# Optimization experiments

Measured on AMD Instinct MI355X. Metric: run time of the kernel, lower is better.

Reference implementation:

```python
import jax, jax.numpy as jnp
import numpy as np


def setup_inputs() -> dict:
    key = jax.random.key(0)
    k1, k2, k3, k4 = jax.random.split(key, 4)
    N, IN, OUT, R, B = 8192, 256, 256, 8, 4
    a = jax.random.normal(k1, (N, N), dtype=jnp.float32)
    x = jax.random.normal(k2, (N, IN, R), dtype=jnp.float32)
    w_bases = jax.random.normal(k3, (B, IN, OUT), dtype=jnp.float32) * (1.0 / np.sqrt(IN))
    w_rel = jax.random.normal(k4, (R, B), dtype=jnp.float32) * 0.5
    return {"a": a, "x": x, "w_bases": w_bases, "w_rel": w_rel}


def reference(a, x, w_bases, w_rel):
    # Basis-combined per-relation weights: [R, IN, OUT]
    w = jnp.einsum('rb,bio->rio', w_rel, w_bases)
    # Per-relation aggregation: support_r = a @ x[:, :, r] -> stack as [N, R, IN]
    # (matches torch.cat([a @ x[:,:,r] for r], dim=1) ordering)
    supports = jnp.einsum('nm,mir->nri', a, x)  # [N, R, IN]
    # tmp [N, R*IN] @ weights [R*IN, OUT] fused as one einsum
    out = jnp.einsum('nri,rio->no', supports, w)  # [N, OUT]
    return out
```

## Files before the change

kernel.cpp:

```cpp
#include <hip/hip_runtime.h>
#include <stdint.h>

typedef __fp16 f16x2 __attribute__((ext_vector_type(2)));
typedef __fp16 f16x8 __attribute__((ext_vector_type(8)));
typedef float  f32x4 __attribute__((ext_vector_type(4)));

#define GLOBAL_AS __attribute__((address_space(1)))
#define LDS_AS    __attribute__((address_space(3)))

#define NN   8192
#define INC  256
#define OUTC 256
#define K2   2048
#define YTN  ((size_t)OUTC * NN)

__device__ __forceinline__ void async_copy16(const void* g, void* l) {
    __builtin_amdgcn_global_load_lds((const GLOBAL_AS uint32_t*)g,
                                     (LDS_AS uint32_t*)l, 16, 0, 0);
}

__device__ __forceinline__ f16x8 cvt_f32x8_to_f16x8(f32x4 u0, f32x4 u1) {
    f16x8 out;
    f16x2* p = (f16x2*)&out;
    p[0] = __builtin_amdgcn_cvt_pkrtz(u0[0], u0[1]);
    p[1] = __builtin_amdgcn_cvt_pkrtz(u0[2], u0[3]);
    p[2] = __builtin_amdgcn_cvt_pkrtz(u1[0], u1[1]);
    p[3] = __builtin_amdgcn_cvt_pkrtz(u1[2], u1[3]);
    return out;
}

__global__ void build_w2t16(const float* __restrict__ wb, const float* __restrict__ wr,
                            __fp16* __restrict__ W2T16) {
    int o = blockIdx.x;
    int i = threadIdx.x;
    float s[8];
#pragma unroll
    for (int r = 0; r < 8; ++r) s[r] = 0.f;
#pragma unroll
    for (int b = 0; b < 4; ++b) {
        float w = wb[((size_t)((b << 8) + i)) * OUTC + o];
#pragma unroll
        for (int r = 0; r < 8; ++r) s[r] = fmaf(wr[r * 4 + b], w, s[r]);
    }
    f16x8 out;
    f16x2* p = (f16x2*)&out;
    p[0] = __builtin_amdgcn_cvt_pkrtz(s[0], s[1]);
    p[1] = __builtin_amdgcn_cvt_pkrtz(s[2], s[3]);
    p[2] = __builtin_amdgcn_cvt_pkrtz(s[4], s[5]);
    p[3] = __builtin_amdgcn_cvt_pkrtz(s[6], s[7]);
    *reinterpret_cast<f16x8*>(&W2T16[(size_t)o * K2 + i * 8]) = out;
}

__global__ __launch_bounds__(256, 2)
void gemm1_xstream(const __fp16* __restrict__ W2, const float* __restrict__ X,
                   float* __restrict__ Cp, int kPerSplit) {
    __shared__ __align__(16) __fp16 As[2][128 * 32];
    const int bm = blockIdx.x * 128;
    const int bn = blockIdx.y * 128;
    const int k0 = blockIdx.z * kPerSplit;

    const int tid  = threadIdx.x;
    const int lane = tid & 63;
    const int wave = tid >> 6;
    const int wm   = (wave >> 1) * 64;
    const int wn   = (wave & 1) * 64;
    const int quad = lane >> 4;
    const int l16  = lane & 15;

    f32x4 acc[4][4];
#pragma unroll
    for (int ti = 0; ti < 4; ++ti)
#pragma unroll
        for (int tj = 0; tj < 4; ++tj)
            acc[ti][tj] = (f32x4){0.f, 0.f, 0.f, 0.f};

    const int nt = kPerSplit / 32;
    int cur = 0;

    {
#pragma unroll
        for (int i = 0; i < 2; ++i) {
            int r0 = wave * 32 + i * 16;
            int r  = r0 + (lane >> 2);
            int c  = (lane & 3) ^ ((r >> 1) & 3);
            async_copy16(W2 + (size_t)(bm + r) * K2 + k0 + c * 8,
                         (char*)As[0] + r0 * 64);
        }
    }

    for (int t = 0; t < nt; ++t) {
        __syncthreads();
        if (t + 1 < nt) {
            int kc = k0 + (t + 1) * 32;
#pragma unroll
            for (int i = 0; i < 2; ++i) {
                int r0 = wave * 32 + i * 16;
                int r  = r0 + (lane >> 2);
                int c  = (lane & 3) ^ ((r >> 1) & 3);
                async_copy16(W2 + (size_t)(bm + r) * K2 + kc + c * 8,
                             (char*)As[cur ^ 1] + r0 * 64);
            }
        }
        const int kc = k0 + t * 32;

        f16x8 bf[4];
#pragma unroll
        for (int j = 0; j < 4; ++j) {
            const float* g = X + (size_t)(bn + wn + j * 16 + l16) * K2 + kc + quad * 8;
            f32x4 u0 = *(const f32x4*)g;
            f32x4 u1 = *(const f32x4*)(g + 4);
            bf[j] = cvt_f32x8_to_f16x8(u0, u1);
        }
        f16x8 af[4];
#pragma unroll
        for (int j = 0; j < 4; ++j) {
            int row = wm + j * 16 + l16;
            int p   = quad ^ ((row >> 1) & 3);
            af[j] = *(const f16x8*)(&As[cur][0] + row * 32 + p * 8);
        }
#pragma unroll
        for (int ti = 0; ti < 4; ++ti)
#pragma unroll
            for (int tj = 0; tj < 4; ++tj)
                acc[ti][tj] = __builtin_amdgcn_mfma_f32_16x16x32_f16(
                    af[ti], bf[tj], acc[ti][tj], 0, 0, 0);
        cur ^= 1;
    }

    float* Cz = Cp + (size_t)blockIdx.z * 256 * NN;
#pragma unroll
    for (int ti = 0; ti < 4; ++ti)
#pragma unroll
        for (int tj = 0; tj < 4; ++tj)
#pragma unroll
            for (int r = 0; r < 4; ++r) {
                int row = bm + wm + ti * 16 + quad * 4 + r;
                int col = bn + wn + tj * 16 + l16;
                Cz[(size_t)row * NN + col] = acc[ti][tj][r];
            }
}

__global__ __launch_bounds__(256, 2)
void gemm2_astream(const float* __restrict__ A, const __fp16* __restrict__ Y,
                   float* __restrict__ Cp, int kPerSplit) {
    __shared__ __align__(16) __fp16 Bs[2][256 * 32];
    const int bm = blockIdx.x * 128;
    const int k0 = blockIdx.z * kPerSplit;

    const int tid  = threadIdx.x;
    const int lane = tid & 63;
    const int wave = tid >> 6;
    const int wm   = (wave >> 1) * 64;
    const int wn   = (wave & 1) * 128;
    const int quad = lane >> 4;
    const int l16  = lane & 15;

    f32x4 acc[4][8];
#pragma unroll
    for (int ti = 0; ti < 4; ++ti)
#pragma unroll
        for (int tj = 0; tj < 8; ++tj)
            acc[ti][tj] = (f32x4){0.f, 0.f, 0.f, 0.f};

    const int nt = kPerSplit / 32;
    int cur = 0;

    {
#pragma unroll
        for (int i = 0; i < 4; ++i) {
            int r0 = wave * 64 + i * 16;
            int r  = r0 + (lane >> 2);
            int c  = (lane & 3) ^ ((r >> 1) & 3);
            async_copy16(Y + (size_t)r * NN + k0 + c * 8,
                         (char*)Bs[0] + r0 * 64);
        }
    }

    for (int t = 0; t < nt; ++t) {
        __syncthreads();
        if (t + 1 < nt) {
            int kc = k0 + (t + 1) * 32;
#pragma unroll
            for (int i = 0; i < 4; ++i) {
                int r0 = wave * 64 + i * 16;
                int r  = r0 + (lane >> 2);
                int c  = (lane & 3) ^ ((r >> 1) & 3);
                async_copy16(Y + (size_t)r * NN + kc + c * 8,
                             (char*)Bs[cur ^ 1] + r0 * 64);
            }
        }
        const int kc = k0 + t * 32;

        f16x8 af[4];
#pragma unroll
        for (int j = 0; j < 4; ++j) {
            const float* g = A + (size_t)(bm + wm + j * 16 + l16) * NN + kc + quad * 8;
            f32x4 u0 = *(const f32x4*)g;
            f32x4 u1 = *(const f32x4*)(g + 4);
            af[j] = cvt_f32x8_to_f16x8(u0, u1);
        }
        f16x8 bf[8];
#pragma unroll
        for (int j = 0; j < 8; ++j) {
            int row = wn + j * 16 + l16;
            int p   = quad ^ ((row >> 1) & 3);
            bf[j] = *(const f16x8*)(&Bs[cur][0] + row * 32 + p * 8);
        }
#pragma unroll
        for (int ti = 0; ti < 4; ++ti)
#pragma unroll
            for (int tj = 0; tj < 8; ++tj)
                acc[ti][tj] = __builtin_amdgcn_mfma_f32_16x16x32_f16(
                    af[ti], bf[tj], acc[ti][tj], 0, 0, 0);
        cur ^= 1;
    }

    float* Cz = Cp + (size_t)blockIdx.z * NN * 256;
#pragma unroll
    for (int ti = 0; ti < 4; ++ti)
#pragma unroll
        for (int tj = 0; tj < 8; ++tj)
#pragma unroll
            for (int r = 0; r < 4; ++r) {
                int row = bm + wm + ti * 16 + quad * 4 + r;
                int col = wn + tj * 16 + l16;
                Cz[(size_t)row * 256 + col] = acc[ti][tj][r];
            }
}

__global__ void reduce_yT(const float* __restrict__ yTp, __fp16* __restrict__ yT16) {
    size_t base = ((size_t)blockIdx.x * 256 + threadIdx.x) * 8;
    f32x4 s0 = (f32x4){0.f, 0.f, 0.f, 0.f};
    f32x4 s1 = (f32x4){0.f, 0.f, 0.f, 0.f};
#pragma unroll
    for (int z = 0; z < 4; ++z) {
        const float* p = yTp + (size_t)z * YTN + base;
        s0 += *(const f32x4*)p;
        s1 += *(const f32x4*)(p + 4);
    }
    *reinterpret_cast<f16x8*>(&yT16[base]) = cvt_f32x8_to_f16x8(s0, s1);
}

__global__ void reduce_out(const float* __restrict__ op, float* __restrict__ out) {
    size_t base = ((size_t)blockIdx.x * 256 + threadIdx.x) * 4;
    f32x4 s = (f32x4){0.f, 0.f, 0.f, 0.f};
#pragma unroll
    for (int z = 0; z < 8; ++z)
        s += *(const f32x4*)(op + (size_t)z * YTN + base);
    *reinterpret_cast<f32x4*>(&out[base]) = s;
}

extern "C" void kernel_launch(void* const* d_in, const int* in_sizes, int n_in,
                              void* d_out, int out_size, void* d_ws, size_t ws_size,
                              hipStream_t stream) {
    const float* a  = (const float*)d_in[0];
    const float* x  = (const float*)d_in[1];
    const float* wb = (const float*)d_in[2];
    const float* wr = (const float*)d_in[3];
    float* out = (float*)d_out;

    char* w = (char*)d_ws;
    float*  yT_p  = (float*)(w);
    __fp16* yT16  = (__fp16*)(w + ((size_t)32 << 20));
    float*  out_p = (float*)(w + ((size_t)36 << 20));
    __fp16* W2T16 = (__fp16*)(w + ((size_t)100 << 20));

    build_w2t16<<<dim3(256), dim3(256), 0, stream>>>(wb, wr, W2T16);

    gemm1_xstream<<<dim3(2, 64, 4), dim3(256), 0, stream>>>(W2T16, x, yT_p, 512);

    reduce_yT<<<dim3(1024), dim3(256), 0, stream>>>(yT_p, yT16);

    gemm2_astream<<<dim3(64, 1, 8), dim3(256), 0, stream>>>(a, yT16, out_p, 1024);

    reduce_out<<<dim3(2048), dim3(256), 0, stream>>>(out_p, out);
}
```

Baseline: 546.2 us.

## Drop LDS staging in both GEMMs, load fragments directly from global memory

Both GEMM kernels stop staging operands in double-buffered shared memory and instead read MFMA fragments straight from global memory with precomputed per-row pointers, which also removes the per-iteration barriers. gemm2's M tile shrinks from 128 to 64 rows, doubling its grid, and both kernels raise their launch-bounds occupancy hint from 2 to 4. The aim is to remove LDS traffic and synchronisation and to hide latency through more resident waves. In exchange, operands that waves used to share through LDS are now fetched separately by each wave, and the fp16 Y matrix is re-read by twice as many blocks in gemm2, which leans on L2.

```diff
diff --git a/kernel.cpp b/kernel.cpp
--- a/kernel.cpp
+++ b/kernel.cpp
@@ -4,20 +4,12 @@
 typedef __fp16 f16x2 __attribute__((ext_vector_type(2)));
 typedef __fp16 f16x8 __attribute__((ext_vector_type(8)));
 typedef float  f32x4 __attribute__((ext_vector_type(4)));
-
-#define GLOBAL_AS __attribute__((address_space(1)))
-#define LDS_AS    __attribute__((address_space(3)))
 
 #define NN   8192
 #define INC  256
 #define OUTC 256
 #define K2   2048
 #define YTN  ((size_t)OUTC * NN)
-
-__device__ __forceinline__ void async_copy16(const void* g, void* l) {
-    __builtin_amdgcn_global_load_lds((const GLOBAL_AS uint32_t*)g,
-                                     (LDS_AS uint32_t*)l, 16, 0, 0);
-}
 
 __device__ __forceinline__ f16x8 cvt_f32x8_to_f16x8(f32x4 u0, f32x4 u1) {
     f16x8 out;
@@ -51,10 +43,9 @@
     *reinterpret_cast<f16x8*>(&W2T16[(size_t)o * K2 + i * 8]) = out;
 }
 
-__global__ __launch_bounds__(256, 2)
-void gemm1_xstream(const __fp16* __restrict__ W2, const float* __restrict__ X,
-                   float* __restrict__ Cp, int kPerSplit) {
-    __shared__ __align__(16) __fp16 As[2][128 * 32];
+__global__ __launch_bounds__(256, 4)
+void gemm1_stream(const __fp16* __restrict__ W2, const float* __restrict__ X,
+                  float* __restrict__ Cp, int kPerSplit) {
     const int bm = blockIdx.x * 128;
     const int bn = blockIdx.y * 128;
     const int k0 = blockIdx.z * kPerSplit;
@@ -74,49 +65,25 @@
         for (int tj = 0; tj < 4; ++tj)
             acc[ti][tj] = (f32x4){0.f, 0.f, 0.f, 0.f};
 
-    const int nt = kPerSplit / 32;
-    int cur = 0;
-
-    {
-#pragma unroll
-        for (int i = 0; i < 2; ++i) {
-            int r0 = wave * 32 + i * 16;
-            int r  = r0 + (lane >> 2);
-            int c  = (lane & 3) ^ ((r >> 1) & 3);
-            async_copy16(W2 + (size_t)(bm + r) * K2 + k0 + c * 8,
-                         (char*)As[0] + r0 * 64);
-        }
-    }
-
-    for (int t = 0; t < nt; ++t) {
-        __syncthreads();
-        if (t + 1 < nt) {
-            int kc = k0 + (t + 1) * 32;
-#pragma unroll
-            for (int i = 0; i < 2; ++i) {
-                int r0 = wave * 32 + i * 16;
-                int r  = r0 + (lane >> 2);
-                int c  = (lane & 3) ^ ((r >> 1) & 3);
-                async_copy16(W2 + (size_t)(bm + r) * K2 + kc + c * 8,
-                             (char*)As[cur ^ 1] + r0 * 64);
-            }
-        }
-        const int kc = k0 + t * 32;
-
+    const __fp16* aptr[4];
+    const float*  bptr[4];
+#pragma unroll
+    for (int j = 0; j < 4; ++j) {
+        aptr[j] = W2 + (size_t)(bm + wm + j * 16 + l16) * K2 + k0 + quad * 8;
+        bptr[j] = X  + (size_t)(bn + wn + j * 16 + l16) * K2 + k0 + quad * 8;
+    }
+
+    for (int kc = 0; kc < kPerSplit; kc += 32) {
+        f16x8 af[4];
         f16x8 bf[4];
 #pragma unroll
+        for (int j = 0; j < 4; ++j)
+            af[j] = *(const f16x8*)(aptr[j] + kc);
+#pragma unroll
         for (int j = 0; j < 4; ++j) {
-            const float* g = X + (size_t)(bn + wn + j * 16 + l16) * K2 + kc + quad * 8;
-            f32x4 u0 = *(const f32x4*)g;
-            f32x4 u1 = *(const f32x4*)(g + 4);
+            f32x4 u0 = *(const f32x4*)(bptr[j] + kc);
+            f32x4 u1 = *(const f32x4*)(bptr[j] + kc + 4);
             bf[j] = cvt_f32x8_to_f16x8(u0, u1);
-        }
-        f16x8 af[4];
-#pragma unroll
-        for (int j = 0; j < 4; ++j) {
-            int row = wm + j * 16 + l16;
-            int p   = quad ^ ((row >> 1) & 3);
-            af[j] = *(const f16x8*)(&As[cur][0] + row * 32 + p * 8);
         }
 #pragma unroll
         for (int ti = 0; ti < 4; ++ti)
@@ -124,7 +91,6 @@
             for (int tj = 0; tj < 4; ++tj)
                 acc[ti][tj] = __builtin_amdgcn_mfma_f32_16x16x32_f16(
                     af[ti], bf[tj], acc[ti][tj], 0, 0, 0);
-        cur ^= 1;
     }
 
     float* Cz = Cp + (size_t)blockIdx.z * 256 * NN;
@@ -140,84 +106,59 @@
             }
 }
 
-__global__ __launch_bounds__(256, 2)
-void gemm2_astream(const float* __restrict__ A, const __fp16* __restrict__ Y,
-                   float* __restrict__ Cp, int kPerSplit) {
-    __shared__ __align__(16) __fp16 Bs[2][256 * 32];
-    const int bm = blockIdx.x * 128;
+__global__ __launch_bounds__(256, 4)
+void gemm2_stream(const float* __restrict__ A, const __fp16* __restrict__ Y,
+                  float* __restrict__ Cp, int kPerSplit) {
+    const int bm = blockIdx.x * 64;
     const int k0 = blockIdx.z * kPerSplit;
 
     const int tid  = threadIdx.x;
     const int lane = tid & 63;
     const int wave = tid >> 6;
-    const int wm   = (wave >> 1) * 64;
+    const int wm   = (wave >> 1) * 32;
     const int wn   = (wave & 1) * 128;
     const int quad = lane >> 4;
     const int l16  = lane & 15;
 
-    f32x4 acc[4][8];
-#pragma unroll
-    for (int ti = 0; ti < 4; ++ti)
+    f32x4 acc[2][8];
+#pragma unroll
+    for (int ti = 0; ti < 2; ++ti)
 #pragma unroll
         for (int tj = 0; tj < 8; ++tj)
             acc[ti][tj] = (f32x4){0.f, 0.f, 0.f, 0.f};
 
-    const int nt = kPerSplit / 32;
-    int cur = 0;
-
-    {
-#pragma unroll
-        for (int i = 0; i < 4; ++i) {
-            int r0 = wave * 64 + i * 16;
-            int r  = r0 + (lane >> 2);
-            int c  = (lane & 3) ^ ((r >> 1) & 3);
-            async_copy16(Y + (size_t)r * NN + k0 + c * 8,
-                         (char*)Bs[0] + r0 * 64);
-        }
-    }
-
-    for (int t = 0; t < nt; ++t) {
-        __syncthreads();
-        if (t + 1 < nt) {
-            int kc = k0 + (t + 1) * 32;
-#pragma unroll
-            for (int i = 0; i < 4; ++i) {
-                int r0 = wave * 64 + i * 16;
-                int r  = r0 + (lane >> 2);
-                int c  = (lane & 3) ^ ((r >> 1) & 3);
-                async_copy16(Y + (size_t)r * NN + kc + c * 8,
-                             (char*)Bs[cur ^ 1] + r0 * 64);
-            }
-        }
-        const int kc = k0 + t * 32;
-
-        f16x8 af[4];
-#pragma unroll
-        for (int j = 0; j < 4; ++j) {
-            const float* g = A + (size_t)(bm + wm + j * 16 + l16) * NN + kc + quad * 8;
-            f32x4 u0 = *(const f32x4*)g;
-            f32x4 u1 = *(const f32x4*)(g + 4);
+    const float*  aptr[2];
+    const __fp16* bptr[8];
+#pragma unroll
+    for (int j = 0; j < 2; ++j)
+        aptr[j] = A + (size_t)(bm + wm + j * 16 + l16) * NN + k0 + quad * 8;
+#pragma unroll
+    for (int j = 0; j < 8; ++j)
+        bptr[j] = Y + (size_t)(wn + j * 16 + l16) * NN + k0 + quad * 8;
+
+    for (int kc = 0; kc < kPerSplit; kc += 32) {
+        f16x8 af[2];
+        f16x8 bf[8];
+#pragma unroll
+        for (int j = 0; j < 2; ++j) {
+            f32x4 u0 = *(const f32x4*)(aptr[j] + kc);
+            f32x4 u1 = *(const f32x4*)(aptr[j] + kc + 4);
             af[j] = cvt_f32x8_to_f16x8(u0, u1);
         }
-        f16x8 bf[8];
-#pragma unroll
-        for (int j = 0; j < 8; ++j) {
-            int row = wn + j * 16 + l16;
-            int p   = quad ^ ((row >> 1) & 3);
-            bf[j] = *(const f16x8*)(&Bs[cur][0] + row * 32 + p * 8);
-        }
-#pragma unroll
-        for (int ti = 0; ti < 4; ++ti)
+#pragma unroll
+        for (int j = 0; j < 8; ++j)
+            bf[j] = *(const f16x8*)(bptr[j] + kc);
+#pragma unroll
+        for (int ti = 0; ti < 2; ++ti)
 #pragma unroll
             for (int tj = 0; tj < 8; ++tj)
                 acc[ti][tj] = __builtin_amdgcn_mfma_f32_16x16x32_f16(
                     af[ti], bf[tj], acc[ti][tj], 0, 0, 0);
-        cur ^= 1;
     }
 
     float* Cz = Cp + (size_t)blockIdx.z * NN * 256;
 #pragma unroll
-    for (int ti = 0; ti < 4; ++ti)
+    for (int ti = 0; ti < 2; ++ti)
 #pragma unroll
         for (int tj = 0; tj < 8; ++tj)
 #pragma unroll
@@ -267,11 +208,11 @@
 
     build_w2t16<<<dim3(256), dim3(256), 0, stream>>>(wb, wr, W2T16);
 
-    gemm1_xstream<<<dim3(2, 64, 4), dim3(256), 0, stream>>>(W2T16, x, yT_p, 512);
+    gemm1_stream<<<dim3(2, 64, 4), dim3(256), 0, stream>>>(W2T16, x, yT_p, 512);
 
     reduce_yT<<<dim3(1024), dim3(256), 0, stream>>>(yT_p, yT16);
 
-    gemm2_astream<<<dim3(64, 1, 8), dim3(256), 0, stream>>>(a, yT16, out_p, 1024);
+    gemm2_stream<<<dim3(128, 1, 8), dim3(256), 0, stream>>>(a, yT16, out_p, 1024);
 
     reduce_out<<<dim3(2048), dim3(256), 0, stream>>>(out_p, out);
 }
```

After: 592.5 us. 1.08x slower.
